# Kernel tuning notes

Hardware: AMD Instinct MI355X
Metric: run time of the kernel (lower is better)

## Reference

```python
import jax, jax.numpy as jnp
import numpy as np

N_NODES = 50000
N_EDGES = 600000
N_GRAPHS = 64
D_IN = 128
D_HID = 128
D_OUT = 64


def setup_inputs() -> dict:
    key = jax.random.key(0)
    ks = jax.random.split(key, 8)
    x = jax.random.normal(ks[0], (N_NODES, D_IN), dtype=jnp.float32)
    edge_index = jax.random.randint(ks[1], (2, N_EDGES), 0, N_NODES, dtype=jnp.int64)
    batch = jnp.sort(jax.random.randint(ks[2], (N_NODES,), 0, N_GRAPHS, dtype=jnp.int64))
    def glorot(k, fan_in, fan_out):
        s = jnp.sqrt(6.0 / (fan_in + fan_out))
        return jax.random.uniform(k, (fan_in, fan_out), jnp.float32, -s, s)
    return {
        "x": x, "edge_index": edge_index, "batch": batch,
        "W1": glorot(ks[3], D_IN, D_HID), "b1": jnp.zeros((D_HID,), jnp.float32),
        "W2": glorot(ks[4], D_HID, D_HID), "b2": jnp.zeros((D_HID,), jnp.float32),
        "W3": glorot(ks[5], D_HID, D_HID), "b3": jnp.zeros((D_HID,), jnp.float32),
        "W4": glorot(ks[6], D_HID, D_OUT), "b4": jnp.zeros((D_OUT,), jnp.float32),
    }


def _gcn_conv(x, W, b, src, dst, deg_inv_sqrt, n_nodes):
    # PyG GCNConv: h = x W; out_i = sum_{j->i} norm_ij h_j  (+ self loop) + b
    h = x @ W  # [N, F]
    norm = deg_inv_sqrt[src] * deg_inv_sqrt[dst]  # [E]
    agg = jax.ops.segment_sum(h[src] * norm[:, None], dst, num_segments=n_nodes)
    # self-loop contribution: norm_ii = deg_inv_sqrt[i]^2
    agg = agg + h * (deg_inv_sqrt * deg_inv_sqrt)[:, None]
    return agg + b


def reference(x, edge_index, batch, W1, b1, W2, b2, W3, b3, W4, b4):
    n = x.shape[0]
    src, dst = edge_index[0], edge_index[1]
    # degree including self loops (PyG add_self_loops + deg over dst)
    deg = jax.ops.segment_sum(jnp.ones_like(dst, dtype=x.dtype), dst, num_segments=n) + 1.0
    deg_inv_sqrt = jax.lax.rsqrt(deg)

    h = jax.nn.relu(_gcn_conv(x, W1, b1, src, dst, deg_inv_sqrt, n))
    h = jax.nn.relu(_gcn_conv(h, W2, b2, src, dst, deg_inv_sqrt, n))
    h = jax.nn.relu(_gcn_conv(h, W3, b3, src, dst, deg_inv_sqrt, n))
    h = _gcn_conv(h, W4, b4, src, dst, deg_inv_sqrt, n)

    # global mean pool over graphs in the batch
    sums = jax.ops.segment_sum(h, batch, num_segments=N_GRAPHS)  # [G, D_OUT]
    cnts = jax.ops.segment_sum(jnp.ones((n,), h.dtype), batch, num_segments=N_GRAPHS)
    hg = sums / jnp.maximum(cnts, 1.0)[:, None]
    return jnp.squeeze(hg)
```

## Files before the change

kernel.cpp:

```cpp
#include <hip/hip_runtime.h>
#include <hip/hip_bf16.h>
#include <hip/hip_fp16.h>

#define N_NODES 50000
#define N_EDGES 600000
#define N_GRAPHS 64
#define PCHUNK 16

typedef __attribute__((ext_vector_type(8))) short bf16x8;
typedef __attribute__((ext_vector_type(4))) float f32x4;

__device__ __forceinline__ unsigned short f2bf(float f) {
    unsigned int u = __float_as_uint(f);
    unsigned int r = u + 0x7fffu + ((u >> 16) & 1u);
    return (unsigned short)(r >> 16);
}
__device__ __forceinline__ float bf_lo(unsigned int u) { return __uint_as_float(u << 16); }
__device__ __forceinline__ float bf_hi(unsigned int u) { return __uint_as_float(u & 0xffff0000u); }
__device__ __forceinline__ float bf1(unsigned short s) {
    return __uint_as_float((unsigned int)s << 16);
}
__device__ __forceinline__ float pnorm(unsigned int e) {
    return __half2float(__ushort_as_half((unsigned short)(e & 0xffffu)));
}

__device__ __forceinline__ void wprep_one(const float* W, unsigned short* Wp, int F, int idx) {
    int i = idx & 7;
    int lane = (idx >> 3) & 63;
    int ks = (idx >> 9) & 3;
    int ct = idx >> 11;
    int k = ks * 32 + (lane >> 4) * 8 + i;
    int col = ct * 16 + (lane & 15);
    Wp[idx] = f2bf(W[(size_t)k * F + col]);
}

__global__ __launch_bounds__(256) void deg_wprep(const int* __restrict__ dst,
                                                 int* __restrict__ degi, int E,
                                                 const float* __restrict__ W1,
                                                 const float* __restrict__ W2,
                                                 const float* __restrict__ W3,
                                                 const float* __restrict__ W4,
                                                 unsigned short* __restrict__ Wp1,
                                                 unsigned short* __restrict__ Wp2,
                                                 unsigned short* __restrict__ Wp3,
                                                 unsigned short* __restrict__ Wp4) {
    const int DEGB = (N_EDGES + 255) / 256;
    int bid = blockIdx.x;
    if (bid < DEGB) {
        int i = bid * 256 + threadIdx.x;
        if (i < E) atomicAdd(&degi[dst[i]], 1);
    } else {
        int wb = bid - DEGB;
        if (wb < 64) wprep_one(W1, Wp1, 128, wb * 256 + threadIdx.x);
        else if (wb < 128) wprep_one(W2, Wp2, 128, (wb - 64) * 256 + threadIdx.x);
        else if (wb < 192) wprep_one(W3, Wp3, 128, (wb - 128) * 256 + threadIdx.x);
        else wprep_one(W4, Wp4, 64, (wb - 192) * 256 + threadIdx.x);
    }
}

__global__ __launch_bounds__(256) void scan_block(const int* __restrict__ in,
                                                  int* __restrict__ excl,
                                                  int* __restrict__ bsum,
                                                  float* __restrict__ dis, int N) {
    __shared__ int s[256];
    int i = blockIdx.x * 256 + threadIdx.x;
    int v = (i < N) ? in[i] : 0;
    s[threadIdx.x] = v;
    __syncthreads();
#pragma unroll
    for (int off = 1; off < 256; off <<= 1) {
        int t = (threadIdx.x >= off) ? s[threadIdx.x - off] : 0;
        __syncthreads();
        s[threadIdx.x] += t;
        __syncthreads();
    }
    if (i < N) {
        excl[i] = s[threadIdx.x] - v;
        dis[i] = rsqrtf((float)v + 1.0f);
    }
    if (threadIdx.x == 255) bsum[blockIdx.x] = s[255];
}

__global__ __launch_bounds__(256) void scan_top(const int* __restrict__ bsum,
                                                int* __restrict__ boff, int NB,
                                                const int* __restrict__ batch,
                                                int* __restrict__ gstart, int N) {
    __shared__ int s[256];
    int v = (threadIdx.x < NB) ? bsum[threadIdx.x] : 0;
    s[threadIdx.x] = v;
    __syncthreads();
#pragma unroll
    for (int off = 1; off < 256; off <<= 1) {
        int t = (threadIdx.x >= off) ? s[threadIdx.x - off] : 0;
        __syncthreads();
        s[threadIdx.x] += t;
        __syncthreads();
    }
    if (threadIdx.x < NB) boff[threadIdx.x] = s[threadIdx.x] - v;

    int g = threadIdx.x;
    if (g <= N_GRAPHS) {
        int lo = 0, hi = N;
        while (lo < hi) {
            int mid = (lo + hi) >> 1;
            if (batch[mid] < g) lo = mid + 1; else hi = mid;
        }
        gstart[g] = lo;
    }
}

__global__ __launch_bounds__(256) void scan_fix(const int* __restrict__ excl,
                                                const int* __restrict__ boff,
                                                int* __restrict__ rowptr,
                                                int* __restrict__ cursor, int N, int E) {
    int i = blockIdx.x * 256 + threadIdx.x;
    if (i < N) {
        int r = excl[i] + boff[blockIdx.x];
        rowptr[i] = r;
        cursor[i] = r;
    }
    if (i == 0) rowptr[N] = E;
}

#define MM1B ((N_NODES + 63) / 64)
#define CSRB ((N_EDGES + 255) / 256)

__global__ __launch_bounds__(256) void csrfill_mm1(const int* __restrict__ src,
                                                   const int* __restrict__ dst,
                                                   const float* __restrict__ dis,
                                                   int* __restrict__ cursor,
                                                   unsigned int* __restrict__ csr, int E,
                                                   const float* __restrict__ Xf,
                                                   const unsigned short* __restrict__ Wp,
                                                   unsigned short* __restrict__ T, int N) {
    if (blockIdx.x >= MM1B) {
        int e = (blockIdx.x - MM1B) * 256 + threadIdx.x;
        if (e >= E) return;
        int s = src[e];
        int d = dst[e];
        float nrm = dis[s] * dis[d];
        unsigned short hb = __half_as_ushort(__float2half(nrm));
        int pos = atomicAdd(&cursor[d], 1);
        csr[pos] = ((unsigned int)s << 16) | (unsigned int)hb;
        return;
    }
    const int lane = threadIdx.x & 63;
    const int wave = threadIdx.x >> 6;
    const int r0 = blockIdx.x * 64 + wave * 16;
    const int kg = lane >> 4;
    const int rdrow = min(r0 + (lane & 15), N - 1);
    const float* xr = Xf + (size_t)rdrow * 128;

    bf16x8 a[4];
#pragma unroll
    for (int ks = 0; ks < 4; ++ks) {
        const int kb = ks * 32 + kg * 8;
        float4 x0 = *reinterpret_cast<const float4*>(xr + kb);
        float4 x1 = *reinterpret_cast<const float4*>(xr + kb + 4);
        float v[8] = {x0.x, x0.y, x0.z, x0.w, x1.x, x1.y, x1.z, x1.w};
#pragma unroll
        for (int i = 0; i < 8; ++i) a[ks][i] = (short)f2bf(v[i]);
    }

#pragma unroll
    for (int ct = 0; ct < 8; ++ct) {
        f32x4 acc = {0.f, 0.f, 0.f, 0.f};
#pragma unroll
        for (int ks = 0; ks < 4; ++ks) {
            bf16x8 b = *reinterpret_cast<const bf16x8*>(Wp + ((size_t)(ct * 4 + ks) * 64 + lane) * 8);
            acc = __builtin_amdgcn_mfma_f32_16x16x32_bf16(a[ks], b, acc, 0, 0, 0);
        }
        const int col = ct * 16 + (lane & 15);
#pragma unroll
        for (int r = 0; r < 4; ++r) {
            const int rowm = r0 + kg * 4 + r;
            if (rowm < N) T[(size_t)rowm * 128 + col] = f2bf(acc[r]);
        }
    }
}

__device__ __forceinline__ void gather128(int beg, int end, const unsigned int* __restrict__ csr,
                                          const unsigned short* __restrict__ T, int lane,
                                          float& ax, float& ay) {
    int p = beg;
    for (; p + 8 <= end; p += 8) {
        unsigned int e0 = csr[p], e1 = csr[p + 1], e2 = csr[p + 2], e3 = csr[p + 3];
        unsigned int e4 = csr[p + 4], e5 = csr[p + 5], e6 = csr[p + 6], e7 = csr[p + 7];
        unsigned int r0 = *reinterpret_cast<const unsigned int*>(T + (size_t)(e0 >> 16) * 128 + lane * 2);
        unsigned int r1 = *reinterpret_cast<const unsigned int*>(T + (size_t)(e1 >> 16) * 128 + lane * 2);
        unsigned int r2 = *reinterpret_cast<const unsigned int*>(T + (size_t)(e2 >> 16) * 128 + lane * 2);
        unsigned int r3 = *reinterpret_cast<const unsigned int*>(T + (size_t)(e3 >> 16) * 128 + lane * 2);
        unsigned int r4 = *reinterpret_cast<const unsigned int*>(T + (size_t)(e4 >> 16) * 128 + lane * 2);
        unsigned int r5 = *reinterpret_cast<const unsigned int*>(T + (size_t)(e5 >> 16) * 128 + lane * 2);
        unsigned int r6 = *reinterpret_cast<const unsigned int*>(T + (size_t)(e6 >> 16) * 128 + lane * 2);
        unsigned int r7 = *reinterpret_cast<const unsigned int*>(T + (size_t)(e7 >> 16) * 128 + lane * 2);
        float n0 = pnorm(e0), n1 = pnorm(e1), n2 = pnorm(e2), n3 = pnorm(e3);
        float n4 = pnorm(e4), n5 = pnorm(e5), n6 = pnorm(e6), n7 = pnorm(e7);
        ax = fmaf(n0, bf_lo(r0), ax); ay = fmaf(n0, bf_hi(r0), ay);
        ax = fmaf(n1, bf_lo(r1), ax); ay = fmaf(n1, bf_hi(r1), ay);
        ax = fmaf(n2, bf_lo(r2), ax); ay = fmaf(n2, bf_hi(r2), ay);
        ax = fmaf(n3, bf_lo(r3), ax); ay = fmaf(n3, bf_hi(r3), ay);
        ax = fmaf(n4, bf_lo(r4), ax); ay = fmaf(n4, bf_hi(r4), ay);
        ax = fmaf(n5, bf_lo(r5), ax); ay = fmaf(n5, bf_hi(r5), ay);
        ax = fmaf(n6, bf_lo(r6), ax); ay = fmaf(n6, bf_hi(r6), ay);
        ax = fmaf(n7, bf_lo(r7), ax); ay = fmaf(n7, bf_hi(r7), ay);
    }
    for (; p + 4 <= end; p += 4) {
        unsigned int e0 = csr[p], e1 = csr[p + 1], e2 = csr[p + 2], e3 = csr[p + 3];
        unsigned int r0 = *reinterpret_cast<const unsigned int*>(T + (size_t)(e0 >> 16) * 128 + lane * 2);
        unsigned int r1 = *reinterpret_cast<const unsigned int*>(T + (size_t)(e1 >> 16) * 128 + lane * 2);
        unsigned int r2 = *reinterpret_cast<const unsigned int*>(T + (size_t)(e2 >> 16) * 128 + lane * 2);
        unsigned int r3 = *reinterpret_cast<const unsigned int*>(T + (size_t)(e3 >> 16) * 128 + lane * 2);
        float n0 = pnorm(e0), n1 = pnorm(e1), n2 = pnorm(e2), n3 = pnorm(e3);
        ax = fmaf(n0, bf_lo(r0), ax); ay = fmaf(n0, bf_hi(r0), ay);
        ax = fmaf(n1, bf_lo(r1), ax); ay = fmaf(n1, bf_hi(r1), ay);
        ax = fmaf(n2, bf_lo(r2), ax); ay = fmaf(n2, bf_hi(r2), ay);
        ax = fmaf(n3, bf_lo(r3), ax); ay = fmaf(n3, bf_hi(r3), ay);
    }
    for (; p < end; ++p) {
        unsigned int e = csr[p];
        float nrm = pnorm(e);
        unsigned int r = *reinterpret_cast<const unsigned int*>(T + (size_t)(e >> 16) * 128 + lane * 2);
        ax = fmaf(nrm, bf_lo(r), ax);
        ay = fmaf(nrm, bf_hi(r), ay);
    }
}

template <int FOUT>
__global__ __launch_bounds__(512) void aggmm(const int* __restrict__ rowptr,
                                             const unsigned int* __restrict__ csr,
                                             const float* __restrict__ dis,
                                             const float* __restrict__ b,
                                             const unsigned short* __restrict__ T,
                                             const unsigned short* __restrict__ Wp,
                                             unsigned short* __restrict__ Tout, int N) {
    __shared__ unsigned short hl[16][136];
    const int lane = threadIdx.x & 63;
    const int wave = threadIdx.x >> 6;
    const int r0 = blockIdx.x * 16;
    const float2 bb = *reinterpret_cast<const float2*>(b + lane * 2);

#pragma unroll 1
    for (int i = 0; i < 2; ++i) {
        const int row = wave * 2 + i;
        const int node = __builtin_amdgcn_readfirstlane(r0 + row);
        if (node >= N) {
            *reinterpret_cast<unsigned int*>(&hl[row][lane * 2]) = 0u;
            continue;
        }
        const int beg = rowptr[node];
        const int end = rowptr[node + 1];
        const float d = dis[node];
        const float d2 = d * d;
        unsigned int selfv =
            *reinterpret_cast<const unsigned int*>(T + (size_t)node * 128 + lane * 2);
        float ax = fmaf(bf_lo(selfv), d2, bb.x);
        float ay = fmaf(bf_hi(selfv), d2, bb.y);
        gather128(beg, end, csr, T, lane, ax, ay);
        unsigned int packed = ((unsigned int)f2bf(ay) << 16) | (unsigned int)f2bf(ax);
        *reinterpret_cast<unsigned int*>(&hl[row][lane * 2]) = packed;
    }
    __syncthreads();

    constexpr int NCT = FOUT / 16;
    if (wave < NCT) {
        const int kg = lane >> 4;
        bf16x8 a[4];
#pragma unroll
        for (int ks = 0; ks < 4; ++ks) {
            bf16x8 av = *reinterpret_cast<const bf16x8*>(&hl[lane & 15][ks * 32 + kg * 8]);
#pragma unroll
            for (int i = 0; i < 8; ++i) av[i] = (av[i] < 0) ? (short)0 : av[i];
            a[ks] = av;
        }

        const int ct = wave;
        f32x4 acc = {0.f, 0.f, 0.f, 0.f};
#pragma unroll
        for (int ks = 0; ks < 4; ++ks) {
            bf16x8 bfr = *reinterpret_cast<const bf16x8*>(Wp + ((size_t)(ct * 4 + ks) * 64 + lane) * 8);
            acc = __builtin_amdgcn_mfma_f32_16x16x32_bf16(a[ks], bfr, acc, 0, 0, 0);
        }
        const int col = ct * 16 + (lane & 15);
#pragma unroll
        for (int r = 0; r < 4; ++r) {
            const int rowm = r0 + kg * 4 + r;
            if (rowm < N) Tout[(size_t)rowm * FOUT + col] = f2bf(acc[r]);
        }
    }
}

__global__ __launch_bounds__(256) void agg64(const int* __restrict__ rowptr,
                                             const unsigned int* __restrict__ csr,
                                             const float* __restrict__ dis,
                                             const float* __restrict__ b,
                                             const unsigned short* __restrict__ T,
                                             unsigned short* __restrict__ H, int N) {
    const int lane = threadIdx.x & 63;
    const int node = __builtin_amdgcn_readfirstlane((blockIdx.x * 256 + threadIdx.x) >> 6);
    if (node >= N) return;

    const int beg = rowptr[node];
    const int end = rowptr[node + 1];
    const float d = dis[node];
    const float d2 = d * d;
    float a = fmaf(bf1(T[(size_t)node * 64 + lane]), d2, b[lane]);

    int p = beg;
    for (; p + 8 <= end; p += 8) {
        unsigned int e0 = csr[p], e1 = csr[p + 1], e2 = csr[p + 2], e3 = csr[p + 3];
        unsigned int e4 = csr[p + 4], e5 = csr[p + 5], e6 = csr[p + 6], e7 = csr[p + 7];
        unsigned short v0 = T[(size_t)(e0 >> 16) * 64 + lane];
        unsigned short v1 = T[(size_t)(e1 >> 16) * 64 + lane];
        unsigned short v2 = T[(size_t)(e2 >> 16) * 64 + lane];
        unsigned short v3 = T[(size_t)(e3 >> 16) * 64 + lane];
        unsigned short v4 = T[(size_t)(e4 >> 16) * 64 + lane];
        unsigned short v5 = T[(size_t)(e5 >> 16) * 64 + lane];
        unsigned short v6 = T[(size_t)(e6 >> 16) * 64 + lane];
        unsigned short v7 = T[(size_t)(e7 >> 16) * 64 + lane];
        a = fmaf(pnorm(e0), bf1(v0), a);
        a = fmaf(pnorm(e1), bf1(v1), a);
        a = fmaf(pnorm(e2), bf1(v2), a);
        a = fmaf(pnorm(e3), bf1(v3), a);
        a = fmaf(pnorm(e4), bf1(v4), a);
        a = fmaf(pnorm(e5), bf1(v5), a);
        a = fmaf(pnorm(e6), bf1(v6), a);
        a = fmaf(pnorm(e7), bf1(v7), a);
    }
    for (; p + 4 <= end; p += 4) {
        unsigned int e0 = csr[p], e1 = csr[p + 1], e2 = csr[p + 2], e3 = csr[p + 3];
        unsigned short v0 = T[(size_t)(e0 >> 16) * 64 + lane];
        unsigned short v1 = T[(size_t)(e1 >> 16) * 64 + lane];
        unsigned short v2 = T[(size_t)(e2 >> 16) * 64 + lane];
        unsigned short v3 = T[(size_t)(e3 >> 16) * 64 + lane];
        a = fmaf(pnorm(e0), bf1(v0), a);
        a = fmaf(pnorm(e1), bf1(v1), a);
        a = fmaf(pnorm(e2), bf1(v2), a);
        a = fmaf(pnorm(e3), bf1(v3), a);
    }
    for (; p < end; ++p) {
        unsigned int e = csr[p];
        a = fmaf(pnorm(e), bf1(T[(size_t)(e >> 16) * 64 + lane]), a);
    }
    H[(size_t)node * 64 + lane] = f2bf(a);
}

__global__ __launch_bounds__(256) void pool_partial(const unsigned short* __restrict__ H,
                                                    const int* __restrict__ gstart,
                                                    float* __restrict__ partial) {
    const int g = blockIdx.x >> 4;
    const int c = blockIdx.x & (PCHUNK - 1);
    const int beg = gstart[g], end = gstart[g + 1];
    const int len = end - beg;
    const int csz = (len + PCHUNK - 1) / PCHUNK;
    const int cb = beg + c * csz;
    const int ce = min(cb + csz, end);
    const int lane = threadIdx.x & 63;
    const int wave = threadIdx.x >> 6;

    float acc = 0.0f;
    for (int n = cb + wave; n < ce; n += 4)
        acc += bf1(H[(size_t)n * 64 + lane]);

    __shared__ float s[4][64];
    s[wave][lane] = acc;
    __syncthreads();
    if (wave == 0)
        partial[(size_t)(g * PCHUNK + c) * 64 + lane] =
            s[0][lane] + s[1][lane] + s[2][lane] + s[3][lane];
}

__global__ __launch_bounds__(64) void pool_fin(const float* __restrict__ partial,
                                               const int* __restrict__ gstart,
                                               float* __restrict__ out) {
    const int g = blockIdx.x;
    const int lane = threadIdx.x;
    float v = 0.0f;
#pragma unroll
    for (int c = 0; c < PCHUNK; ++c) v += partial[(size_t)(g * PCHUNK + c) * 64 + lane];
    float cnt = (float)(gstart[g + 1] - gstart[g]);
    out[g * 64 + lane] = v / fmaxf(cnt, 1.0f);
}

extern "C" void kernel_launch(void* const* d_in, const int* in_sizes, int n_in,
                              void* d_out, int out_size, void* d_ws, size_t ws_size,
                              hipStream_t stream) {
    const float* x = (const float*)d_in[0];
    const int* ei = (const int*)d_in[1];
    const int* batch = (const int*)d_in[2];
    const float* W1 = (const float*)d_in[3];
    const float* b1 = (const float*)d_in[4];
    const float* W2 = (const float*)d_in[5];
    const float* b2 = (const float*)d_in[6];
    const float* W3 = (const float*)d_in[7];
    const float* b3 = (const float*)d_in[8];
    const float* W4 = (const float*)d_in[9];
    const float* b4 = (const float*)d_in[10];

    const int N = N_NODES, E = N_EDGES;
    const int* src = ei;
    const int* dst = ei + E;

    char* base = (char*)d_ws;
    size_t off = 0;
    auto carve = [&](size_t bytes) -> void* {
        off = (off + 63) & ~(size_t)63;
        void* p = base + off;
        off += bytes;
        return p;
    };
    unsigned short* Ta = (unsigned short*)carve((size_t)N * 128 * 2);
    unsigned short* Tb = (unsigned short*)carve((size_t)N * 128 * 2);
    unsigned short* H = (unsigned short*)carve((size_t)N * 64 * 2);
    int* degi = (int*)carve((size_t)N * 4);
    float* dis = (float*)carve((size_t)N * 4);
    int* rowptr = (int*)carve((size_t)(N + 1) * 4);
    int* cursor = (int*)carve((size_t)N * 4);
    int* excl = (int*)carve((size_t)N * 4);
    int* bsum = (int*)carve(256 * 4);
    int* boff = (int*)carve(256 * 4);
    unsigned int* csr = (unsigned int*)carve((size_t)E * 4);
    int* gstart = (int*)carve(65 * 4);
    float* partial = (float*)carve((size_t)N_GRAPHS * PCHUNK * 64 * 4);
    unsigned short* Wp1 = (unsigned short*)carve(128 * 128 * 2);
    unsigned short* Wp2 = (unsigned short*)carve(128 * 128 * 2);
    unsigned short* Wp3 = (unsigned short*)carve(128 * 128 * 2);
    unsigned short* Wp4 = (unsigned short*)carve(128 * 64 * 2);

    hipMemsetAsync(degi, 0, N * sizeof(int), stream);

    const int NB = (N + 255) / 256;
    const int DEGB = (E + 255) / 256;
    deg_wprep<<<DEGB + 224, 256, 0, stream>>>(dst, degi, E, W1, W2, W3, W4,
                                              Wp1, Wp2, Wp3, Wp4);
    scan_block<<<NB, 256, 0, stream>>>(degi, excl, bsum, dis, N);
    scan_top<<<1, 256, 0, stream>>>(bsum, boff, NB, batch, gstart, N);
    scan_fix<<<NB, 256, 0, stream>>>(excl, boff, rowptr, cursor, N, E);
    csrfill_mm1<<<MM1B + CSRB, 256, 0, stream>>>(src, dst, dis, cursor, csr, E,
                                                 x, Wp1, Ta, N);

    const int FUS = (N + 15) / 16;

    aggmm<128><<<FUS, 512, 0, stream>>>(rowptr, csr, dis, b1, Ta, Wp2, Tb, N);
    aggmm<128><<<FUS, 512, 0, stream>>>(rowptr, csr, dis, b2, Tb, Wp3, Ta, N);
    aggmm<64><<<FUS, 512, 0, stream>>>(rowptr, csr, dis, b3, Ta, Wp4, Tb, N);
    agg64<<<(N * 64 + 255) / 256, 256, 0, stream>>>(rowptr, csr, dis, b4, Tb, H, N);

    pool_partial<<<N_GRAPHS * PCHUNK, 256, 0, stream>>>(H, gstart, partial);
    pool_fin<<<N_GRAPHS, 64, 0, stream>>>(partial, gstart, (float*)d_out);
}
```

Measured before the change: 193.2 us.

## Aggregate two adjacent nodes per wave and partition CSR fill by destination range

The aggregation kernels now have each wave handle two consecutive nodes as one contiguous CSR range. Edges are routed to one of two accumulators by comparing their position against the middle row pointer, which removes the per-row loop and its tail and evens out load across the wave. The CSR fill launches eight times as many edge blocks, each keeping only edges whose destination falls in its eighth of the node range. This is meant to localize atomic and scatter traffic, at the cost of reading src/dst eight times. Bounds checks were dropped because N is a multiple of 16, which ties correctness to the fixed sizes.

```diff
diff --git a/kernel.cpp b/kernel.cpp
--- a/kernel.cpp
+++ b/kernel.cpp
@@ -134,10 +134,13 @@
                                                    const unsigned short* __restrict__ Wp,
                                                    unsigned short* __restrict__ T, int N) {
     if (blockIdx.x >= MM1B) {
-        int e = (blockIdx.x - MM1B) * 256 + threadIdx.x;
+        const int part = blockIdx.x & 7;
+        const int ch = (blockIdx.x - MM1B) >> 3;
+        int e = ch * 256 + threadIdx.x;
         if (e >= E) return;
+        int d = dst[e];
+        if ((d * 8) / N_NODES != part) return;
         int s = src[e];
-        int d = dst[e];
         float nrm = dis[s] * dis[d];
         unsigned short hb = __half_as_ushort(__float2half(nrm));
         int pos = atomicAdd(&cursor[d], 1);
@@ -179,9 +182,10 @@
     }
 }
 
-__device__ __forceinline__ void gather128(int beg, int end, const unsigned int* __restrict__ csr,
-                                          const unsigned short* __restrict__ T, int lane,
-                                          float& ax, float& ay) {
+__device__ __forceinline__ void gather128x2(int beg, int mid, int end,
+                                            const unsigned int* __restrict__ csr,
+                                            const unsigned short* __restrict__ T, int lane,
+                                            float& ax0, float& ay0, float& ax1, float& ay1) {
     int p = beg;
     for (; p + 8 <= end; p += 8) {
         unsigned int e0 = csr[p], e1 = csr[p + 1], e2 = csr[p + 2], e3 = csr[p + 3];
@@ -194,16 +198,16 @@
         unsigned int r5 = *reinterpret_cast<const unsigned int*>(T + (size_t)(e5 >> 16) * 128 + lane * 2);
         unsigned int r6 = *reinterpret_cast<const unsigned int*>(T + (size_t)(e6 >> 16) * 128 + lane * 2);
         unsigned int r7 = *reinterpret_cast<const unsigned int*>(T + (size_t)(e7 >> 16) * 128 + lane * 2);
-        float n0 = pnorm(e0), n1 = pnorm(e1), n2 = pnorm(e2), n3 = pnorm(e3);
-        float n4 = pnorm(e4), n5 = pnorm(e5), n6 = pnorm(e6), n7 = pnorm(e7);
-        ax = fmaf(n0, bf_lo(r0), ax); ay = fmaf(n0, bf_hi(r0), ay);
-        ax = fmaf(n1, bf_lo(r1), ax); ay = fmaf(n1, bf_hi(r1), ay);
-        ax = fmaf(n2, bf_lo(r2), ax); ay = fmaf(n2, bf_hi(r2), ay);
-        ax = fmaf(n3, bf_lo(r3), ax); ay = fmaf(n3, bf_hi(r3), ay);
-        ax = fmaf(n4, bf_lo(r4), ax); ay = fmaf(n4, bf_hi(r4), ay);
-        ax = fmaf(n5, bf_lo(r5), ax); ay = fmaf(n5, bf_hi(r5), ay);
-        ax = fmaf(n6, bf_lo(r6), ax); ay = fmaf(n6, bf_hi(r6), ay);
-        ax = fmaf(n7, bf_lo(r7), ax); ay = fmaf(n7, bf_hi(r7), ay);
+#define ACC8(K)                                                                  \
+        {                                                                        \
+            float n = pnorm(e##K);                                               \
+            float na = (p + K < mid) ? n : 0.0f;                                 \
+            float nb = (p + K < mid) ? 0.0f : n;                                 \
+            ax0 = fmaf(na, bf_lo(r##K), ax0); ay0 = fmaf(na, bf_hi(r##K), ay0);  \
+            ax1 = fmaf(nb, bf_lo(r##K), ax1); ay1 = fmaf(nb, bf_hi(r##K), ay1);  \
+        }
+        ACC8(0) ACC8(1) ACC8(2) ACC8(3) ACC8(4) ACC8(5) ACC8(6) ACC8(7)
+#undef ACC8
     }
     for (; p + 4 <= end; p += 4) {
         unsigned int e0 = csr[p], e1 = csr[p + 1], e2 = csr[p + 2], e3 = csr[p + 3];
@@ -211,18 +215,25 @@
         unsigned int r1 = *reinterpret_cast<const unsigned int*>(T + (size_t)(e1 >> 16) * 128 + lane * 2);
         unsigned int r2 = *reinterpret_cast<const unsigned int*>(T + (size_t)(e2 >> 16) * 128 + lane * 2);
         unsigned int r3 = *reinterpret_cast<const unsigned int*>(T + (size_t)(e3 >> 16) * 128 + lane * 2);
-        float n0 = pnorm(e0), n1 = pnorm(e1), n2 = pnorm(e2), n3 = pnorm(e3);
-        ax = fmaf(n0, bf_lo(r0), ax); ay = fmaf(n0, bf_hi(r0), ay);
-        ax = fmaf(n1, bf_lo(r1), ax); ay = fmaf(n1, bf_hi(r1), ay);
-        ax = fmaf(n2, bf_lo(r2), ax); ay = fmaf(n2, bf_hi(r2), ay);
-        ax = fmaf(n3, bf_lo(r3), ax); ay = fmaf(n3, bf_hi(r3), ay);
+#define ACC4(K)                                                                  \
+        {                                                                        \
+            float n = pnorm(e##K);                                               \
+            float na = (p + K < mid) ? n : 0.0f;                                 \
+            float nb = (p + K < mid) ? 0.0f : n;                                 \
+            ax0 = fmaf(na, bf_lo(r##K), ax0); ay0 = fmaf(na, bf_hi(r##K), ay0);  \
+            ax1 = fmaf(nb, bf_lo(r##K), ax1); ay1 = fmaf(nb, bf_hi(r##K), ay1);  \
+        }
+        ACC4(0) ACC4(1) ACC4(2) ACC4(3)
+#undef ACC4
     }
     for (; p < end; ++p) {
         unsigned int e = csr[p];
-        float nrm = pnorm(e);
         unsigned int r = *reinterpret_cast<const unsigned int*>(T + (size_t)(e >> 16) * 128 + lane * 2);
-        ax = fmaf(nrm, bf_lo(r), ax);
-        ay = fmaf(nrm, bf_hi(r), ay);
+        float n = pnorm(e);
+        float na = (p < mid) ? n : 0.0f;
+        float nb = (p < mid) ? 0.0f : n;
+        ax0 = fmaf(na, bf_lo(r), ax0); ay0 = fmaf(na, bf_hi(r), ay0);
+        ax1 = fmaf(nb, bf_lo(r), ax1); ay1 = fmaf(nb, bf_hi(r), ay1);
     }
 }
 
@@ -240,26 +251,25 @@
     const int r0 = blockIdx.x * 16;
     const float2 bb = *reinterpret_cast<const float2*>(b + lane * 2);
 
-#pragma unroll 1
-    for (int i = 0; i < 2; ++i) {
-        const int row = wave * 2 + i;
-        const int node = __builtin_amdgcn_readfirstlane(r0 + row);
-        if (node >= N) {
-            *reinterpret_cast<unsigned int*>(&hl[row][lane * 2]) = 0u;
-            continue;
-        }
-        const int beg = rowptr[node];
-        const int end = rowptr[node + 1];
-        const float d = dis[node];
-        const float d2 = d * d;
-        unsigned int selfv =
-            *reinterpret_cast<const unsigned int*>(T + (size_t)node * 128 + lane * 2);
-        float ax = fmaf(bf_lo(selfv), d2, bb.x);
-        float ay = fmaf(bf_hi(selfv), d2, bb.y);
-        gather128(beg, end, csr, T, lane, ax, ay);
-        unsigned int packed = ((unsigned int)f2bf(ay) << 16) | (unsigned int)f2bf(ax);
-        *reinterpret_cast<unsigned int*>(&hl[row][lane * 2]) = packed;
-    }
+    const int n0 = __builtin_amdgcn_readfirstlane(r0 + wave * 2);
+    const int beg = rowptr[n0];
+    const int mid = rowptr[n0 + 1];
+    const int end = rowptr[n0 + 2];
+    const float d0 = dis[n0], d1 = dis[n0 + 1];
+
+    unsigned int s0 = *reinterpret_cast<const unsigned int*>(T + (size_t)n0 * 128 + lane * 2);
+    unsigned int s1 = *reinterpret_cast<const unsigned int*>(T + (size_t)(n0 + 1) * 128 + lane * 2);
+    float ax0 = fmaf(bf_lo(s0), d0 * d0, bb.x);
+    float ay0 = fmaf(bf_hi(s0), d0 * d0, bb.y);
+    float ax1 = fmaf(bf_lo(s1), d1 * d1, bb.x);
+    float ay1 = fmaf(bf_hi(s1), d1 * d1, bb.y);
+
+    gather128x2(beg, mid, end, csr, T, lane, ax0, ay0, ax1, ay1);
+
+    *reinterpret_cast<unsigned int*>(&hl[wave * 2 + 0][lane * 2]) =
+        ((unsigned int)f2bf(ay0) << 16) | (unsigned int)f2bf(ax0);
+    *reinterpret_cast<unsigned int*>(&hl[wave * 2 + 1][lane * 2]) =
+        ((unsigned int)f2bf(ay1) << 16) | (unsigned int)f2bf(ax1);
     __syncthreads();
 
     constexpr int NCT = FOUT / 16;
@@ -284,8 +294,7 @@
         const int col = ct * 16 + (lane & 15);
 #pragma unroll
         for (int r = 0; r < 4; ++r) {
-            const int rowm = r0 + kg * 4 + r;
-            if (rowm < N) Tout[(size_t)rowm * FOUT + col] = f2bf(acc[r]);
+            Tout[(size_t)(r0 + kg * 4 + r) * FOUT + col] = f2bf(acc[r]);
         }
     }
 }
@@ -297,14 +306,16 @@
                                              const unsigned short* __restrict__ T,
                                              unsigned short* __restrict__ H, int N) {
     const int lane = threadIdx.x & 63;
-    const int node = __builtin_amdgcn_readfirstlane((blockIdx.x * 256 + threadIdx.x) >> 6);
-    if (node >= N) return;
-
-    const int beg = rowptr[node];
-    const int end = rowptr[node + 1];
-    const float d = dis[node];
-    const float d2 = d * d;
-    float a = fmaf(bf1(T[(size_t)node * 64 + lane]), d2, b[lane]);
+    const int n0 = __builtin_amdgcn_readfirstlane(((blockIdx.x * 256 + threadIdx.x) >> 6) * 2);
+    if (n0 >= N) return;
+
+    const int beg = rowptr[n0];
+    const int mid = rowptr[n0 + 1];
+    const int end = rowptr[n0 + 2];
+    const float d0 = dis[n0], d1 = dis[n0 + 1];
+    const float blane = b[lane];
+    float a0 = fmaf(bf1(T[(size_t)n0 * 64 + lane]), d0 * d0, blane);
+    float a1 = fmaf(bf1(T[(size_t)(n0 + 1) * 64 + lane]), d1 * d1, blane);
 
     int p = beg;
     for (; p + 8 <= end; p += 8) {
@@ -318,31 +329,28 @@
         unsigned short v5 = T[(size_t)(e5 >> 16) * 64 + lane];
         unsigned short v6 = T[(size_t)(e6 >> 16) * 64 + lane];
         unsigned short v7 = T[(size_t)(e7 >> 16) * 64 + lane];
-        a = fmaf(pnorm(e0), bf1(v0), a);
-        a = fmaf(pnorm(e1), bf1(v1), a);
-        a = fmaf(pnorm(e2), bf1(v2), a);
-        a = fmaf(pnorm(e3), bf1(v3), a);
-        a = fmaf(pnorm(e4), bf1(v4), a);
-        a = fmaf(pnorm(e5), bf1(v5), a);
-        a = fmaf(pnorm(e6), bf1(v6), a);
-        a = fmaf(pnorm(e7), bf1(v7), a);
-    }
-    for (; p + 4 <= end; p += 4) {
-        unsigned int e0 = csr[p], e1 = csr[p + 1], e2 = csr[p + 2], e3 = csr[p + 3];
-        unsigned short v0 = T[(size_t)(e0 >> 16) * 64 + lane];
-        unsigned short v1 = T[(size_t)(e1 >> 16) * 64 + lane];
-        unsigned short v2 = T[(size_t)(e2 >> 16) * 64 + lane];
-        unsigned short v3 = T[(size_t)(e3 >> 16) * 64 + lane];
-        a = fmaf(pnorm(e0), bf1(v0), a);
-        a = fmaf(pnorm(e1), bf1(v1), a);
-        a = fmaf(pnorm(e2), bf1(v2), a);
-        a = fmaf(pnorm(e3), bf1(v3), a);
+#define A64(K)                                                       \
+        {                                                            \
+            float n = pnorm(e##K);                                   \
+            float na = (p + K < mid) ? n : 0.0f;                     \
+            float nb = (p + K < mid) ? 0.0f : n;                     \
+            a0 = fmaf(na, bf1(v##K), a0);                            \
+            a1 = fmaf(nb, bf1(v##K), a1);                            \
+        }
+        A64(0) A64(1) A64(2) A64(3) A64(4) A64(5) A64(6) A64(7)
+#undef A64
     }
     for (; p < end; ++p) {
         unsigned int e = csr[p];
-        a = fmaf(pnorm(e), bf1(T[(size_t)(e >> 16) * 64 + lane]), a);
-    }
-    H[(size_t)node * 64 + lane] = f2bf(a);
+        unsigned short v = T[(size_t)(e >> 16) * 64 + lane];
+        float n = pnorm(e);
+        float na = (p < mid) ? n : 0.0f;
+        float nb = (p < mid) ? 0.0f : n;
+        a0 = fmaf(na, bf1(v), a0);
+        a1 = fmaf(nb, bf1(v), a1);
+    }
+    H[(size_t)n0 * 64 + lane] = f2bf(a0);
+    H[(size_t)(n0 + 1) * 64 + lane] = f2bf(a1);
 }
 
 __global__ __launch_bounds__(256) void pool_partial(const unsigned short* __restrict__ H,
@@ -436,15 +444,15 @@
     scan_block<<<NB, 256, 0, stream>>>(degi, excl, bsum, dis, N);
     scan_top<<<1, 256, 0, stream>>>(bsum, boff, NB, batch, gstart, N);
     scan_fix<<<NB, 256, 0, stream>>>(excl, boff, rowptr, cursor, N, E);
-    csrfill_mm1<<<MM1B + CSRB, 256, 0, stream>>>(src, dst, dis, cursor, csr, E,
-                                                 x, Wp1, Ta, N);
+    csrfill_mm1<<<MM1B + 8 * CSRB, 256, 0, stream>>>(src, dst, dis, cursor, csr, E,
+                                                     x, Wp1, Ta, N);
 
     const int FUS = (N + 15) / 16;
 
     aggmm<128><<<FUS, 512, 0, stream>>>(rowptr, csr, dis, b1, Ta, Wp2, Tb, N);
     aggmm<128><<<FUS, 512, 0, stream>>>(rowptr, csr, dis, b2, Tb, Wp3, Ta, N);
     aggmm<64><<<FUS, 512, 0, stream>>>(rowptr, csr, dis, b3, Ta, Wp4, Tb, N);
-    agg64<<<(N * 64 + 255) / 256, 256, 0, stream>>>(rowptr, csr, dis, b4, Tb, H, N);
+    agg64<<<(N / 2 * 64 + 255) / 256, 256, 0, stream>>>(rowptr, csr, dis, b4, Tb, H, N);
 
     pool_partial<<<N_GRAPHS * PCHUNK, 256, 0, stream>>>(H, gstart, partial);
     pool_fin<<<N_GRAPHS, 64, 0, stream>>>(partial, gstart, (float*)d_out);
```

After: 181.8 us. 5.9% less time.
